# Optimization experiments

Hardware: AMD Instinct MI355X
Metric: run time of the kernel (lower is better)

The kernel has to match this reference:

```python
import jax, jax.numpy as jnp
import numpy as np

EMBED_DIM = 300
HIDDEN = 128
N_CLS = 20
N_NODES = 100000
N_EDGES = 1600000
N_GRAPHS = 512
EPSILON = 1e-06


def setup_inputs() -> dict:
    key = jax.random.key(0)
    ks = jax.random.split(key, 10)
    x_fp16 = jax.random.normal(ks[0], (N_NODES, EMBED_DIM), dtype=jnp.float16)
    ei = jax.random.randint(ks[1], (2, N_EDGES), 0, N_NODES, dtype=jnp.int32)
    batch = jnp.sort(jax.random.randint(ks[2], (N_NODES,), 0, N_GRAPHS, dtype=jnp.int32))
    mask = jax.random.randint(ks[3], (N_NODES,), 0, 2, dtype=jnp.int32).astype(jnp.bool_)
    def glorot(k, fan_in, fan_out):
        s = (6.0 / (fan_in + fan_out)) ** 0.5
        return jax.random.uniform(k, (fan_in, fan_out), jnp.float32, -s, s)
    return {
        "x_fp16": x_fp16, "ei": ei, "batch": batch, "mask": mask,
        "W1": glorot(ks[4], EMBED_DIM, HIDDEN), "b1": jnp.zeros((HIDDEN,), jnp.float32),
        "W2": glorot(ks[5], HIDDEN, HIDDEN), "b2": jnp.zeros((HIDDEN,), jnp.float32),
        "Wout": glorot(ks[6], HIDDEN, N_CLS), "bout": jnp.zeros((N_CLS,), jnp.float32),
    }


def gcn_conv(x, W, b, src, dst, n):
    # PyG GCNConv: x' = D^{-1/2} (A + I) D^{-1/2} (x W) + b
    h = x @ W  # [N, out]
    loop = jnp.arange(n, dtype=src.dtype)
    s = jnp.concatenate([src, loop])
    d = jnp.concatenate([dst, loop])
    deg = jax.ops.segment_sum(jnp.ones_like(d, dtype=h.dtype), d, num_segments=n)
    dinv = jax.lax.rsqrt(deg)  # deg >= 1 thanks to self-loops
    norm = dinv[s] * dinv[d]  # [E+N]
    msg = h[s] * norm[:, None]
    return jax.ops.segment_sum(msg, d, num_segments=n) + b


def reference(x_fp16, ei, batch, mask, W1, b1, W2, b2, Wout, bout):
    n = x_fp16.shape[0]
    src, dst = ei[0], ei[1]
    x = x_fp16.astype(jnp.float32)
    x = jax.nn.relu(gcn_conv(x, W1, b1, src, dst, n))
    x = jax.nn.relu(gcn_conv(x, W2, b2, src, dst, n))
    m = mask.astype(jnp.float32)[:, None]  # [N,1]
    ent_sum = jax.ops.segment_sum(x * m, batch, num_segments=N_GRAPHS)  # [G,H]
    ent_cnt = jax.ops.segment_sum(m, batch, num_segments=N_GRAPHS)  # [G,1]
    doc_vec = ent_sum / (ent_cnt + EPSILON)
    # fallback: mean over all nodes when a graph has no masked entities
    node_sum = jax.ops.segment_sum(x, batch, num_segments=N_GRAPHS)
    node_cnt = jax.ops.segment_sum(jnp.ones((n, 1), jnp.float32), batch, num_segments=N_GRAPHS)
    mean_pool = node_sum / jnp.maximum(node_cnt, 1.0)
    zero = ent_cnt < EPSILON  # [G,1]
    doc_vec = jnp.where(zero, mean_pool, doc_vec)
    return jax.nn.log_softmax(doc_vec @ Wout + bout, axis=1)
```

## Files before the change

kernel.cpp:

```cpp
#include <hip/hip_runtime.h>
#include <hip/hip_fp16.h>

#define NN 100000
#define NE 1600000
#define DIM 300
#define HID 128
#define NC 20
#define NG 512
#define NBK 196
#define BCH 4096

typedef _Float16 h8 __attribute__((ext_vector_type(8)));
typedef float f4 __attribute__((ext_vector_type(4)));

union pack16 { float4 v; __half2 h2[4]; };

__device__ __forceinline__ __half tohalf(float v) {
  if (!(v == v)) v = 0.f;
  v = fminf(fmaxf(v, -60000.f), 60000.f);
  return __float2half(v);
}

__device__ __forceinline__ float load_x(const void* xraw, size_t o, int mode) {
  float v;
  if (mode == 2) v = ((const float*)xraw)[o];
  else {
    unsigned short u = ((const unsigned short*)xraw)[o];
    if (mode == 1) { union { unsigned w; float f; } c; c.w = ((unsigned)u) << 16; v = c.f; }
    else { union { unsigned short s; _Float16 h; } c; c.s = u; v = (float)c.h; }
  }
  if (!(v == v)) v = 0.f;
  return fminf(fmaxf(v, -1e4f), 1e4f);
}

__device__ __forceinline__ void cvt4(const void* Ain, size_t off, int mode, _Float16* o) {
  if (mode == 2) {
    float4 fv = *(const float4*)((const float*)Ain + off);
    o[0] = (_Float16)fv.x; o[1] = (_Float16)fv.y; o[2] = (_Float16)fv.z; o[3] = (_Float16)fv.w;
  } else {
    uint2 u = *(const uint2*)((const unsigned short*)Ain + off);
    unsigned short s0 = u.x & 0xFFFF, s1 = u.x >> 16, s2 = u.y & 0xFFFF, s3 = u.y >> 16;
    if (mode == 1) {
      union { unsigned w; float f; } c0, c1, c2, c3;
      c0.w = ((unsigned)s0) << 16; c1.w = ((unsigned)s1) << 16;
      c2.w = ((unsigned)s2) << 16; c3.w = ((unsigned)s3) << 16;
      o[0] = (_Float16)c0.f; o[1] = (_Float16)c1.f; o[2] = (_Float16)c2.f; o[3] = (_Float16)c3.f;
    } else {
      union { unsigned short s; _Float16 h; } d0, d1, d2, d3;
      d0.s = s0; d1.s = s1; d2.s = s2; d3.s = s3;
      o[0] = d0.h; o[1] = d1.h; o[2] = d2.h; o[3] = d3.h;
    }
  }
}


__global__ void k_probe(const unsigned short* __restrict__ xu,
                        const unsigned* __restrict__ Araw, const unsigned* __restrict__ Braw,
                        const int* __restrict__ e32,
                        const float* __restrict__ W1, const float* __restrict__ W2,
                        _Float16* __restrict__ w1f, _Float16* __restrict__ w2f,
                        unsigned* __restrict__ diag) {
  int b = blockIdx.x, t = threadIdx.x;
  if (b < 96) {
    int mode = b % 3, chunk = b / 3;
    float m = 0.f;
    if (mode == 0) {
      int base = chunk * 16384;
      for (int j = t; j < 16384; j += 256) {
        union { unsigned short s; _Float16 h; } c; c.s = xu[base + j];
        float v = fabsf((float)c.h);
        if (v == v && v < 65000.f) m = fmaxf(m, v);
      }
    } else if (mode == 1) {
      int base = chunk * 16384;
      for (int j = t; j < 16384; j += 256) {
        union { unsigned w; float f; } c; c.w = ((unsigned)xu[base + j]) << 16;
        float v = fabsf(c.f);
        if (v == v && v < 1e30f) m = fmaxf(m, v);
      }
    } else {
      const float* xf = (const float*)xu;
      int base = chunk * 8192;
      for (int j = t; j < 8192; j += 256) {
        float v = fabsf(xf[base + j]);
        if (v == v && v < 1e30f) m = fmaxf(m, v);
      }
    }
    for (int off = 32; off; off >>= 1) m = fmaxf(m, __shfl_xor(m, off));
    if ((t & 63) == 0) atomicMax(&diag[20 + mode], __float_as_uint(m));
  } else if (b == 96 || b == 97) {
    __shared__ unsigned red[256];
    const unsigned* p = (b == 96) ? Araw : Braw;
    unsigned m = 0;
    for (int j = t; j < 25000; j += 256) m = max(m, p[j]);
    red[t] = m; __syncthreads();
    for (int off = 128; off; off >>= 1) { if (t < off) red[t] = max(red[t], red[t + off]); __syncthreads(); }
    if (t == 0) diag[(b == 96) ? 24 : 25] = red[0];
  } else if (b < 102) {
    int i = (b - 98) * 256 + t;
    unsigned z = 0;
    for (; i < 50000; i += 1024) if (e32[2 * i + 1] == 0) z++;
    for (int off = 32; off; off >>= 1) z += __shfl_xor(z, off);
    if ((t & 63) == 0) atomicAdd(&diag[26], z);
  } else {
    int idx = (b - 102) * 256 + t;
    const int S1 = 10 * 8 * 64 * 8;
    const int S2 = 4 * 8 * 64 * 8;
    if (idx < S1) {
      int j = idx & 7, l = (idx >> 3) & 63, nt = (idx >> 9) & 7, kc = idx >> 12;
      int k = kc * 32 + ((l >> 4) << 3) + j;
      int n = nt * 16 + (l & 15);
      w1f[idx] = (k < DIM) ? (_Float16)W1[k * HID + n] : (_Float16)0.f;
    } else if (idx < S1 + S2) {
      int q = idx - S1;
      int j = q & 7, l = (q >> 3) & 63, nt = (q >> 9) & 7, kc = q >> 12;
      int k = kc * 32 + ((l >> 4) << 3) + j;
      int n = nt * 16 + (l & 15);
      w2f[q] = (_Float16)W2[k * HID + n];
    }
  }
}


__global__ void k_setup(const unsigned* __restrict__ diag, int* __restrict__ flags,
                        const int* __restrict__ A, const int* __restrict__ B,
                        int* __restrict__ bcnt, int* __restrict__ gstart) {
  __shared__ int sflags[8];
  int t = threadIdx.x;
  if (t == 0) {
    float M16 = __uint_as_float(diag[20]);
    float M32 = __uint_as_float(diag[21]);
    float Mf  = __uint_as_float(diag[22]);
    int xmode = 3;
    if      (Mf  > 3.f && Mf  < 8.f) xmode = 2;
    else if (M32 > 3.f && M32 < 8.f) xmode = 1;
    else if (M16 > 3.f && M16 < 8.f) xmode = 0;
    unsigned uA = diag[24], uB = diag[25];
    bool Ab = (uA >= 32u && uA < 1024u), Bb = (uB >= 32u && uB < 1024u);
    int swap = -1;
    if (Ab && !Bb) swap = 0;
    else if (Bb && !Ab) swap = 1;
    int mint = -1;
    if (swap >= 0) {
      unsigned um = (swap == 0) ? uB : uA;
      if (um <= 1u) mint = 1;
      else if (um >= 65536u) mint = 0;
    }
    sflags[0] = xmode;
    sflags[1] = (mint == 1) ? 1 : 0;
    sflags[2] = (swap == 1) ? 1 : 0;
    sflags[3] = (diag[26] >= 49990u) ? 1 : 0;
    sflags[4] = (swap >= 0 && mint >= 0) ? 1 : 0;
    #pragma unroll
    for (int j = 0; j < 5; j++) flags[j] = sflags[j];
  }
  __syncthreads();
  const int* batch = sflags[2] ? B : A;
  if (t <= NG) {
    if (t == NG) gstart[NG] = NN;
    else {
      int lo = 0, hi = NN;
      while (lo < hi) { int mid = (lo + hi) >> 1; if (batch[mid] < t) lo = mid + 1; else hi = mid; }
      gstart[t] = lo;
    }
  }
  if (t < NBK) bcnt[t] = 0;
}


__global__ void k_bhist(const int* __restrict__ e32, const int* __restrict__ flags,
                        int* __restrict__ bcnt) {
  __shared__ int hist[NBK];
  int e64 = flags[3];
  int t = threadIdx.x;
  for (int j = t; j < NBK; j += 256) hist[j] = 0;
  __syncthreads();
  int i = blockIdx.x * blockDim.x + t;
  int stride = gridDim.x * blockDim.x;
  for (; i < NE; i += stride) {
    int s = e64 ? e32[2 * i] : e32[i];
    int d = e64 ? e32[2 * NE + 2 * i] : e32[NE + i];
    if ((unsigned)s < (unsigned)NN && (unsigned)d < (unsigned)NN)
      atomicAdd(&hist[d >> 9], 1);
  }
  __syncthreads();
  for (int j = t; j < NBK; j += 256) if (hist[j]) atomicAdd(&bcnt[j], hist[j]);
}

__global__ void k_bscan(const int* __restrict__ bcnt, int* __restrict__ boff,
                        int* __restrict__ bcur) {
  if (blockIdx.x == 0 && threadIdx.x == 0) {
    int run = 0;
    for (int j = 0; j < NBK; j++) { boff[j] = run; bcur[j] = run; run += bcnt[j]; }
    boff[NBK] = run;
  }
}

__global__ __launch_bounds__(256)
void k_bscatter(const int* __restrict__ e32, const int* __restrict__ flags,
                int* __restrict__ bcur, unsigned* __restrict__ ebuf) {
  __shared__ uint2 stage[BCH];
  __shared__ int hist[NBK];
  __shared__ int lbase[NBK];
  __shared__ int lcur[NBK];
  int e64 = flags[3];
  int t = threadIdx.x;
  for (int j = t; j < NBK; j += 256) { hist[j] = 0; lcur[j] = 0; }
  __syncthreads();
  int start = blockIdx.x * BCH;
  int n = NE - start; if (n > BCH) n = BCH;
  for (int i = t; i < n; i += 256) {
    int idx = start + i;
    int s = e64 ? e32[2 * idx] : e32[idx];
    int d = e64 ? e32[2 * NE + 2 * idx] : e32[NE + idx];
    bool ok = ((unsigned)s < (unsigned)NN) && ((unsigned)d < (unsigned)NN);
    stage[i] = make_uint2(ok ? (unsigned)s : 0xFFFFFFFFu, (unsigned)(ok ? d : 0));
    if (ok) atomicAdd(&hist[d >> 9], 1);
  }
  __syncthreads();
  for (int j = t; j < NBK; j += 256) if (hist[j] > 0) lbase[j] = atomicAdd(&bcur[j], hist[j]);
  __syncthreads();
  for (int i = t; i < n; i += 256) {
    unsigned s = stage[i].x;
    if (s == 0xFFFFFFFFu) continue;
    int d = (int)stage[i].y;
    int b = d >> 9;
    int o = atomicAdd(&lcur[b], 1);
    ebuf[lbase[b] + o] = (s << 9) | (unsigned)(d & 511);
  }
}

__global__ __launch_bounds__(256)
void k_bfinal(const unsigned* __restrict__ ebuf, const int* __restrict__ boff,
              int* __restrict__ row_off, float* __restrict__ dinv, int* __restrict__ csr) {
  __shared__ int ldeg[512];
  __shared__ int lcur[512];
  int b = blockIdx.x, t = threadIdx.x;
  int base = b * 512;
  int nn = NN - base; if (nn > 512) nn = 512;
  for (int j = t; j < 512; j += 256) ldeg[j] = 0;
  __syncthreads();
  int s0 = boff[b], s1 = boff[b + 1];
  for (int e = s0 + t; e < s1; e += 256) atomicAdd(&ldeg[ebuf[e] & 511], 1);
  __syncthreads();
  if (t == 0) {
    int run = s0;
    for (int i = 0; i < nn; i++) { lcur[i] = run; row_off[base + i] = run; run += ldeg[i]; }
    if (b == gridDim.x - 1) row_off[NN] = run;
  }
  __syncthreads();
  for (int j = t; j < nn; j += 256) dinv[base + j] = rsqrtf((float)ldeg[j] + 1.0f);
  for (int e = s0 + t; e < s1; e += 256) {
    unsigned v = ebuf[e];
    int p = atomicAdd(&lcur[v & 511], 1);
    csr[p] = (int)(v >> 9);
  }
}


#define XS1 168

__global__ __launch_bounds__(512)
void k_gemm1_mfma(const void* __restrict__ Ain, const _Float16* __restrict__ bfrag,
                  const float* __restrict__ dinv, const int* __restrict__ flags,
                  __half* __restrict__ outg) {
  __shared__ _Float16 xs[64 * XS1];
  const int mode = flags[0] & 3;
  int tid = threadIdx.x;
  int w = tid >> 6, l = tid & 63;
  int rowbase = blockIdx.x * 64;
  int k0base = (l >> 4) << 3;
  int cb = l & 15;

  f4 acc[4];
  f4 zero = {0.f, 0.f, 0.f, 0.f};
  #pragma unroll
  for (int rg = 0; rg < 4; rg++) acc[rg] = zero;

  #pragma unroll
  for (int it = 0; it < 5; it++) {
    int c = tid + it * 512;
    int rl = c / 40, kk = (c - rl * 40) * 4;
    int r = rowbase + rl;
    _Float16 o[4] = {0, 0, 0, 0};
    if (r < NN) cvt4(Ain, (size_t)r * DIM + kk, mode, o);
    _Float16* p = &xs[rl * XS1 + kk];
    p[0] = o[0]; p[1] = o[1]; p[2] = o[2]; p[3] = o[3];
  }
  __syncthreads();
  #pragma unroll
  for (int kc = 0; kc < 5; kc++) {
    int ko = kc * 32 + k0base;
    h8 a0 = *(const h8*)&xs[(0 * 16 + cb) * XS1 + ko];
    h8 a1 = *(const h8*)&xs[(1 * 16 + cb) * XS1 + ko];
    h8 a2 = *(const h8*)&xs[(2 * 16 + cb) * XS1 + ko];
    h8 a3 = *(const h8*)&xs[(3 * 16 + cb) * XS1 + ko];
    h8 bv = *(const h8*)&bfrag[(((kc << 3) + w) * 64 + l) * 8];
    acc[0] = __builtin_amdgcn_mfma_f32_16x16x32_f16(a0, bv, acc[0], 0, 0, 0);
    acc[1] = __builtin_amdgcn_mfma_f32_16x16x32_f16(a1, bv, acc[1], 0, 0, 0);
    acc[2] = __builtin_amdgcn_mfma_f32_16x16x32_f16(a2, bv, acc[2], 0, 0, 0);
    acc[3] = __builtin_amdgcn_mfma_f32_16x16x32_f16(a3, bv, acc[3], 0, 0, 0);
  }
  __syncthreads();

  for (int t2 = tid; t2 < 64 * 10; t2 += 512) {
    int rl = t2 / 10, j = t2 - rl * 10;
    *(unsigned*)&xs[rl * XS1 + 140 + j * 2] = 0u;
  }
  #pragma unroll
  for (int it = 0; it < 5; it++) {
    int c = tid + it * 512;
    if (c < 64 * 35) {
      int rl = c / 35, kk = (c - rl * 35) * 4;
      int r = rowbase + rl;
      _Float16 o[4] = {0, 0, 0, 0};
      if (r < NN) cvt4(Ain, (size_t)r * DIM + 160 + kk, mode, o);
      _Float16* p = &xs[rl * XS1 + kk];
      p[0] = o[0]; p[1] = o[1]; p[2] = o[2]; p[3] = o[3];
    }
  }
  __syncthreads();
  #pragma unroll
  for (int kc = 5; kc < 10; kc++) {
    int ko = (kc - 5) * 32 + k0base;
    h8 a0 = *(const h8*)&xs[(0 * 16 + cb) * XS1 + ko];
    h8 a1 = *(const h8*)&xs[(1 * 16 + cb) * XS1 + ko];
    h8 a2 = *(const h8*)&xs[(2 * 16 + cb) * XS1 + ko];
    h8 a3 = *(const h8*)&xs[(3 * 16 + cb) * XS1 + ko];
    h8 bv = *(const h8*)&bfrag[(((kc << 3) + w) * 64 + l) * 8];
    acc[0] = __builtin_amdgcn_mfma_f32_16x16x32_f16(a0, bv, acc[0], 0, 0, 0);
    acc[1] = __builtin_amdgcn_mfma_f32_16x16x32_f16(a1, bv, acc[1], 0, 0, 0);
    acc[2] = __builtin_amdgcn_mfma_f32_16x16x32_f16(a2, bv, acc[2], 0, 0, 0);
    acc[3] = __builtin_amdgcn_mfma_f32_16x16x32_f16(a3, bv, acc[3], 0, 0, 0);
  }

  int rquad = (l >> 4) << 2;
  #pragma unroll
  for (int rg = 0; rg < 4; rg++) {
    #pragma unroll
    for (int i = 0; i < 4; i++) {
      int r = rowbase + rg * 16 + rquad + i;
      if (r >= NN) continue;
      float dv = dinv[r];
      outg[(size_t)r * HID + w * 16 + cb] = tohalf(acc[rg][i] * dv);
    }
  }
}


__global__ __launch_bounds__(256)
void k_gemm2_mfma(const __half* __restrict__ Ain, const _Float16* __restrict__ bfrag,
                  const float* __restrict__ dinv, __half* __restrict__ outg) {
  __shared__ _Float16 xs[64 * 136];
  int tid = threadIdx.x;
  int w = tid >> 6, l = tid & 63;
  int rowbase = blockIdx.x * 64;
  int k0base = (l >> 4) << 3;
  int cb = l & 15;

  {
    h8 regs[4];
    #pragma unroll
    for (int it = 0; it < 4; it++) {
      int c = tid + it * 256;
      int rl = c >> 4, k = (c & 15) * 8;
      int r = rowbase + rl;
      h8 v = {};
      if (r < NN) v = *(const h8*)((const _Float16*)Ain + (size_t)r * HID + k);
      regs[it] = v;
    }
    __builtin_amdgcn_sched_barrier(0);
    #pragma unroll
    for (int it = 0; it < 4; it++) {
      int c = tid + it * 256;
      int rl = c >> 4, k = (c & 15) * 8;
      *(h8*)&xs[rl * 136 + k] = regs[it];
    }
  }
  __syncthreads();

  f4 acc[4][2];
  f4 zero = {0.f, 0.f, 0.f, 0.f};
  #pragma unroll
  for (int rg = 0; rg < 4; rg++) { acc[rg][0] = zero; acc[rg][1] = zero; }

  #pragma unroll
  for (int kc = 0; kc < 4; kc++) {
    int ko = kc * 32 + k0base;
    h8 a0 = *(const h8*)&xs[(0 * 16 + cb) * 136 + ko];
    h8 a1 = *(const h8*)&xs[(1 * 16 + cb) * 136 + ko];
    h8 a2 = *(const h8*)&xs[(2 * 16 + cb) * 136 + ko];
    h8 a3 = *(const h8*)&xs[(3 * 16 + cb) * 136 + ko];
    #pragma unroll
    for (int ntl = 0; ntl < 2; ntl++) {
      int nt = w * 2 + ntl;
      h8 bv = *(const h8*)&bfrag[(((kc << 3) + nt) * 64 + l) * 8];
      acc[0][ntl] = __builtin_amdgcn_mfma_f32_16x16x32_f16(a0, bv, acc[0][ntl], 0, 0, 0);
      acc[1][ntl] = __builtin_amdgcn_mfma_f32_16x16x32_f16(a1, bv, acc[1][ntl], 0, 0, 0);
      acc[2][ntl] = __builtin_amdgcn_mfma_f32_16x16x32_f16(a2, bv, acc[2][ntl], 0, 0, 0);
      acc[3][ntl] = __builtin_amdgcn_mfma_f32_16x16x32_f16(a3, bv, acc[3][ntl], 0, 0, 0);
    }
  }

  int rquad = (l >> 4) << 2;
  #pragma unroll
  for (int rg = 0; rg < 4; rg++) {
    #pragma unroll
    for (int i = 0; i < 4; i++) {
      int r = rowbase + rg * 16 + rquad + i;
      if (r >= NN) continue;
      float dv = dinv[r];
      __half* orow = outg + (size_t)r * HID;
      orow[(w * 2 + 0) * 16 + cb] = tohalf(acc[rg][0][i] * dv);
      orow[(w * 2 + 1) * 16 + cb] = tohalf(acc[rg][1][i] * dv);
    }
  }
}


__global__ __launch_bounds__(256)
void k_agg(const __half* __restrict__ g, const float* __restrict__ dinv,
           const int* __restrict__ row_off, const int* __restrict__ csr,
           const float* __restrict__ bias, __half* __restrict__ out) {
  int tid = threadIdx.x;
  int node = blockIdx.x * 4 + (tid >> 6);
  int l = tid & 63;
  if (node >= NN) return;
  int grp = l >> 4;
  int cl  = l & 15;
  size_t coff = (size_t)cl * 8;

  float a0 = 0.f, a1 = 0.f, a2 = 0.f, a3 = 0.f, a4 = 0.f, a5 = 0.f, a6 = 0.f, a7 = 0.f;
  pack16 r;

  #define ACCUM() do { \
    float2 f0 = __half22float2(r.h2[0]); \
    float2 f1 = __half22float2(r.h2[1]); \
    float2 f2 = __half22float2(r.h2[2]); \
    float2 f3 = __half22float2(r.h2[3]); \
    a0 += f0.x; a1 += f0.y; a2 += f1.x; a3 += f1.y; \
    a4 += f2.x; a5 += f2.y; a6 += f3.x; a7 += f3.y; } while (0)

  int e0 = row_off[node], e1 = row_off[node + 1];
  int e = e0 + grp;
  for (; e + 4 < e1; e += 8) {
    int s1 = csr[e], s2 = csr[e + 4];
    pack16 rA, rB;
    rA.v = *(const float4*)(g + (size_t)s1 * HID + coff);
    rB.v = *(const float4*)(g + (size_t)s2 * HID + coff);
    r = rA; ACCUM();
    r = rB; ACCUM();
  }
  if (e < e1) {
    int s1 = csr[e];
    r.v = *(const float4*)(g + (size_t)s1 * HID + coff);
    ACCUM();
  }
  if (grp == 0) {
    r.v = *(const float4*)(g + (size_t)node * HID + coff);
    ACCUM();
  }
  #undef ACCUM

  a0 += __shfl_xor(a0, 16); a1 += __shfl_xor(a1, 16); a2 += __shfl_xor(a2, 16); a3 += __shfl_xor(a3, 16);
  a4 += __shfl_xor(a4, 16); a5 += __shfl_xor(a5, 16); a6 += __shfl_xor(a6, 16); a7 += __shfl_xor(a7, 16);
  a0 += __shfl_xor(a0, 32); a1 += __shfl_xor(a1, 32); a2 += __shfl_xor(a2, 32); a3 += __shfl_xor(a3, 32);
  a4 += __shfl_xor(a4, 32); a5 += __shfl_xor(a5, 32); a6 += __shfl_xor(a6, 32); a7 += __shfl_xor(a7, 32);

  if (grp == 0) {
    float di = dinv[node];
    const float* bp = bias + coff;
    pack16 w;
    w.h2[0] = __floats2half2_rn(fmaxf(a0 * di + bp[0], 0.f), fmaxf(a1 * di + bp[1], 0.f));
    w.h2[1] = __floats2half2_rn(fmaxf(a2 * di + bp[2], 0.f), fmaxf(a3 * di + bp[3], 0.f));
    w.h2[2] = __floats2half2_rn(fmaxf(a4 * di + bp[4], 0.f), fmaxf(a5 * di + bp[5], 0.f));
    w.h2[3] = __floats2half2_rn(fmaxf(a6 * di + bp[6], 0.f), fmaxf(a7 * di + bp[7], 0.f));
    *(float4*)(out + (size_t)node * HID + coff) = w.v;
  }
}


__global__ __launch_bounds__(256)
void k_pool(const __half* __restrict__ o2, const void* __restrict__ Araw, const void* __restrict__ Braw,
            const int* __restrict__ gstart, const int* __restrict__ flags,
            float* __restrict__ doc) {
  __shared__ float lex[4][HID];
  __shared__ float lnx[4][HID];
  __shared__ int lec[4];
  int gid = blockIdx.x, tid = threadIdx.x;
  int wv = tid >> 6, l = tid & 63;
  int grp = l >> 4, cl = l & 15;
  size_t coff = (size_t)cl * 8;
  const int mint = flags[1];
  const void* mraw = flags[2] ? Araw : Braw;
  const unsigned char* m8 = (const unsigned char*)mraw;
  const int* m32 = (const int*)mraw;
  int s = gstart[gid], e = gstart[gid + 1];

  float ex[8], nx[8];
  #pragma unroll
  for (int j = 0; j < 8; j++) { ex[j] = 0.f; nx[j] = 0.f; }
  int ec = 0;

  for (int n = s + wv * 4 + grp; n < e; n += 16) {
    pack16 r;
    r.v = *(const float4*)(o2 + (size_t)n * HID + coff);
    float2 f0 = __half22float2(r.h2[0]);
    float2 f1 = __half22float2(r.h2[1]);
    float2 f2 = __half22float2(r.h2[2]);
    float2 f3 = __half22float2(r.h2[3]);
    float t0 = f0.x, t1 = f0.y, t2 = f1.x, t3 = f1.y;
    float t4 = f2.x, t5 = f2.y, t6 = f3.x, t7 = f3.y;
    nx[0] += t0; nx[1] += t1; nx[2] += t2; nx[3] += t3;
    nx[4] += t4; nx[5] += t5; nx[6] += t6; nx[7] += t7;
    bool mv = mint ? (m32[n] != 0) : (m8[n] != 0);
    if (mv) {
      ex[0] += t0; ex[1] += t1; ex[2] += t2; ex[3] += t3;
      ex[4] += t4; ex[5] += t5; ex[6] += t6; ex[7] += t7;
      ec++;
    }
  }
  #pragma unroll
  for (int j = 0; j < 8; j++) {
    ex[j] += __shfl_xor(ex[j], 16); ex[j] += __shfl_xor(ex[j], 32);
    nx[j] += __shfl_xor(nx[j], 16); nx[j] += __shfl_xor(nx[j], 32);
  }
  ec += __shfl_xor(ec, 16); ec += __shfl_xor(ec, 32);

  if (grp == 0) {
    #pragma unroll
    for (int j = 0; j < 8; j++) { lex[wv][cl * 8 + j] = ex[j]; lnx[wv][cl * 8 + j] = nx[j]; }
    if (cl == 0) lec[wv] = ec;
  }
  __syncthreads();
  if (tid < HID) {
    float exT = lex[0][tid] + lex[1][tid] + lex[2][tid] + lex[3][tid];
    float nxT = lnx[0][tid] + lnx[1][tid] + lnx[2][tid] + lnx[3][tid];
    int ecT = lec[0] + lec[1] + lec[2] + lec[3];
    int cnt = e - s;
    float dv;
    if (ecT > 0) dv = exT / ((float)ecT + 1e-6f);
    else dv = (cnt > 0) ? nxT / (float)cnt : 0.f;
    doc[gid * HID + tid] = dv;
  }
}

__global__ __launch_bounds__(64)
void k_out(const float* __restrict__ doc, const float* __restrict__ Wout,
           const float* __restrict__ bout, float* __restrict__ out) {
  __shared__ float dv[HID];
  int gid = blockIdx.x, l = threadIdx.x;
  dv[l] = doc[gid * HID + l];
  dv[l + 64] = doc[gid * HID + l + 64];
  __syncthreads();
  float logit = -1e30f;
  if (l < NC) {
    float acc = bout[l];
    for (int k = 0; k < HID; k++) acc += dv[k] * Wout[k * NC + l];
    logit = acc;
  }
  float m = logit;
  for (int off = 32; off; off >>= 1) m = fmaxf(m, __shfl_xor(m, off));
  float ex = (l < NC) ? expf(logit - m) : 0.f;
  float ssum = ex;
  for (int off = 32; off; off >>= 1) ssum += __shfl_xor(ssum, off);
  if (l < NC) out[gid * NC + l] = (logit - m) - logf(ssum);
}

__global__ void k_fail(float* __restrict__ out, float enc) {
  int i = blockIdx.x * blockDim.x + threadIdx.x;
  if (i < NG * NC) out[i] = -enc;
}


extern "C" void kernel_launch(void* const* d_in, const int* in_sizes, int n_in,
                              void* d_out, int out_size, void* d_ws, size_t ws_size,
                              hipStream_t stream) {
  int ix = -1, iei = -1, iA = -1, iB = -1, iW1 = -1, ib1 = -1, iW2 = -1, ib2 = -1, iWo = -1, ibo = -1;
  for (int i = 0; i < n_in; i++) {
    int s = in_sizes[i];
    if (s == 30000000) ix = i;
    else if (s == 3200000) iei = i;
    else if (s == 100000) { if (iA < 0) iA = i; else iB = i; }
    else if (s == 38400) iW1 = i;
    else if (s == 16384) iW2 = i;
    else if (s == 2560) iWo = i;
    else if (s == 20) ibo = i;
    else if (s == 128) { if (ib1 < 0) ib1 = i; else ib2 = i; }
  }
  float* out = (float*)d_out;
  int miss = -1;
  if (ix < 0) miss = 0; else if (iei < 0) miss = 1; else if (iA < 0 || iB < 0) miss = 2;
  else if (iW1 < 0) miss = 3; else if (ib1 < 0 || ib2 < 0) miss = 4; else if (iW2 < 0) miss = 5;
  else if (iWo < 0) miss = 6; else if (ibo < 0) miss = 7;
  if (miss >= 0) {
    k_fail<<<(NG * NC + 255) / 256, 256, 0, stream>>>(out, 8192.f + 64.f * (float)miss);
    return;
  }
  const void* x = d_in[ix];
  const int* e32 = (const int*)d_in[iei];
  const void* Araw = d_in[iA];
  const void* Braw = d_in[iB];
  const float* W1 = (const float*)d_in[iW1];
  const float* b1 = (const float*)d_in[ib1];
  const float* W2 = (const float*)d_in[iW2];
  const float* b2 = (const float*)d_in[ib2];
  const float* Wout = (const float*)d_in[iWo];
  const float* bout = (const float*)d_in[ibo];

  char* ws = (char*)d_ws;
  size_t off = 0;
  auto alloc = [&](size_t bytes) -> char* {
    char* p = ws + off; off += (bytes + 255) & ~(size_t)255; return p;
  };
  float* dinv   = (float*)alloc((size_t)NN * 4);
  int* row_off  = (int*)alloc((size_t)(NN + 1) * 4);
  int* csr      = (int*)alloc((size_t)NE * 4);
  int* bcnt     = (int*)alloc((size_t)NBK * 4);
  int* boff     = (int*)alloc((size_t)(NBK + 1) * 4);
  int* bcur     = (int*)alloc((size_t)NBK * 4);
  int* gstart   = (int*)alloc((size_t)(NG + 1) * 4);
  int* flags    = (int*)alloc(8 * 4);
  _Float16* w1f = (_Float16*)alloc(40960 * 2);
  _Float16* w2f = (_Float16*)alloc(16384 * 2);
  __half* gbuf  = (__half*)alloc((size_t)NN * HID * 2);
  __half* obuf  = (__half*)alloc((size_t)NN * HID * 2);
  float* doc    = (float*)alloc((size_t)NG * HID * 4);
  unsigned* diag = (unsigned*)alloc(64 * 4);
  unsigned* ebuf = (unsigned*)gbuf;

  hipMemsetAsync(diag, 0, 64 * 4, stream);

  k_probe<<<326, 256, 0, stream>>>((const unsigned short*)x, (const unsigned*)Araw,
                                   (const unsigned*)Braw, e32, W1, W2, w1f, w2f, diag);
  k_setup<<<1, 576, 0, stream>>>(diag, flags, (const int*)Araw, (const int*)Braw, bcnt, gstart);

  k_bhist<<<1024, 256, 0, stream>>>(e32, flags, bcnt);
  k_bscan<<<1, 64, 0, stream>>>(bcnt, boff, bcur);
  k_bscatter<<<(NE + BCH - 1) / BCH, 256, 0, stream>>>(e32, flags, bcur, ebuf);
  k_bfinal<<<NBK, 256, 0, stream>>>(ebuf, boff, row_off, dinv, csr);

  k_gemm1_mfma<<<(NN + 63) / 64, 512, 0, stream>>>(x, w1f, dinv, flags, gbuf);
  k_agg<<<NN / 4, 256, 0, stream>>>(gbuf, dinv, row_off, csr, b1, obuf);
  k_gemm2_mfma<<<(NN + 63) / 64, 256, 0, stream>>>(obuf, w2f, dinv, gbuf);
  k_agg<<<NN / 4, 256, 0, stream>>>(gbuf, dinv, row_off, csr, b2, obuf);

  k_pool<<<NG, 256, 0, stream>>>(obuf, Araw, Braw, gstart, flags, doc);
  k_out<<<NG, 64, 0, stream>>>(doc, Wout, bout, out);
}
```

Measured before the change: 309.0 us.

## Fuse layer-1 aggregation into GEMM2, fold scan into histogram, fuse pooling with output head

The first aggregation now runs inside the GEMM2 kernel: each 64-row block gathers neighbour features into shared memory and then runs the MFMA tiles from there, so the aggregated layer-1 activations are never written to or re-read from global memory. The bucket prefix scan moves into the last finishing block of the histogram kernel, coordinated by an atomic counter. The pooling and classifier/log-softmax kernels are merged. Together these drop three launches and one full intermediate round trip, but the fused kernel has only about 1563 blocks doing irregular gathers, which may lower parallelism and latency hiding compared with the separate aggregation kernel.

```diff
diff --git a/kernel.cpp b/kernel.cpp
--- a/kernel.cpp
+++ b/kernel.cpp
@@ -169,7 +169,8 @@
 
 
 __global__ void k_bhist(const int* __restrict__ e32, const int* __restrict__ flags,
-                        int* __restrict__ bcnt) {
+                        int* __restrict__ bcnt, int* __restrict__ boff,
+                        int* __restrict__ bcur, unsigned* __restrict__ done) {
   __shared__ int hist[NBK];
   int e64 = flags[3];
   int t = threadIdx.x;
@@ -185,14 +186,14 @@
   }
   __syncthreads();
   for (int j = t; j < NBK; j += 256) if (hist[j]) atomicAdd(&bcnt[j], hist[j]);
-}
-
-__global__ void k_bscan(const int* __restrict__ bcnt, int* __restrict__ boff,
-                        int* __restrict__ bcur) {
-  if (blockIdx.x == 0 && threadIdx.x == 0) {
-    int run = 0;
-    for (int j = 0; j < NBK; j++) { boff[j] = run; bcur[j] = run; run += bcnt[j]; }
-    boff[NBK] = run;
+  __threadfence();
+  __syncthreads();
+  if (t == 0) {
+    if (atomicAdd(done, 1u) == gridDim.x - 1) {
+      int run = 0;
+      for (int j = 0; j < NBK; j++) { boff[j] = run; bcur[j] = run; run += bcnt[j]; }
+      boff[NBK] = run;
+    }
   }
 }
 
@@ -349,36 +350,78 @@
 
 
 __global__ __launch_bounds__(256)
-void k_gemm2_mfma(const __half* __restrict__ Ain, const _Float16* __restrict__ bfrag,
-                  const float* __restrict__ dinv, __half* __restrict__ outg) {
+void k_aggemm2(const __half* __restrict__ g, const float* __restrict__ dinv,
+               const int* __restrict__ row_off, const int* __restrict__ csr,
+               const float* __restrict__ bias, const _Float16* __restrict__ bfrag,
+               __half* __restrict__ outg) {
   __shared__ _Float16 xs[64 * 136];
   int tid = threadIdx.x;
   int w = tid >> 6, l = tid & 63;
   int rowbase = blockIdx.x * 64;
+  int grp = l >> 4;
+  int cl  = l & 15;
+  size_t coff = (size_t)cl * 8;
+
+  for (int it = 0; it < 16; it++) {
+    int nloc = it * 4 + w;
+    int node = rowbase + nloc;
+    float a0 = 0.f, a1 = 0.f, a2 = 0.f, a3 = 0.f, a4 = 0.f, a5 = 0.f, a6 = 0.f, a7 = 0.f;
+    pack16 r;
+
+    #define ACCUM() do { \
+      float2 f0 = __half22float2(r.h2[0]); \
+      float2 f1 = __half22float2(r.h2[1]); \
+      float2 f2 = __half22float2(r.h2[2]); \
+      float2 f3 = __half22float2(r.h2[3]); \
+      a0 += f0.x; a1 += f0.y; a2 += f1.x; a3 += f1.y; \
+      a4 += f2.x; a5 += f2.y; a6 += f3.x; a7 += f3.y; } while (0)
+
+    int e0 = 0, e1 = 0;
+    if (node < NN) { e0 = row_off[node]; e1 = row_off[node + 1]; }
+    int e = e0 + grp;
+    for (; e + 4 < e1; e += 8) {
+      int s1 = csr[e], s2 = csr[e + 4];
+      pack16 rA, rB;
+      rA.v = *(const float4*)(g + (size_t)s1 * HID + coff);
+      rB.v = *(const float4*)(g + (size_t)s2 * HID + coff);
+      r = rA; ACCUM();
+      r = rB; ACCUM();
+    }
+    if (e < e1) {
+      int s1 = csr[e];
+      r.v = *(const float4*)(g + (size_t)s1 * HID + coff);
+      ACCUM();
+    }
+    if (grp == 0 && node < NN) {
+      r.v = *(const float4*)(g + (size_t)node * HID + coff);
+      ACCUM();
+    }
+    #undef ACCUM
+
+    a0 += __shfl_xor(a0, 16); a1 += __shfl_xor(a1, 16); a2 += __shfl_xor(a2, 16); a3 += __shfl_xor(a3, 16);
+    a4 += __shfl_xor(a4, 16); a5 += __shfl_xor(a5, 16); a6 += __shfl_xor(a6, 16); a7 += __shfl_xor(a7, 16);
+    a0 += __shfl_xor(a0, 32); a1 += __shfl_xor(a1, 32); a2 += __shfl_xor(a2, 32); a3 += __shfl_xor(a3, 32);
+    a4 += __shfl_xor(a4, 32); a5 += __shfl_xor(a5, 32); a6 += __shfl_xor(a6, 32); a7 += __shfl_xor(a7, 32);
+
+    if (grp == 0) {
+      pack16 wv;
+      if (node < NN) {
+        float di = dinv[node];
+        const float* bp = bias + coff;
+        wv.h2[0] = __floats2half2_rn(fmaxf(a0 * di + bp[0], 0.f), fmaxf(a1 * di + bp[1], 0.f));
+        wv.h2[1] = __floats2half2_rn(fmaxf(a2 * di + bp[2], 0.f), fmaxf(a3 * di + bp[3], 0.f));
+        wv.h2[2] = __floats2half2_rn(fmaxf(a4 * di + bp[4], 0.f), fmaxf(a5 * di + bp[5], 0.f));
+        wv.h2[3] = __floats2half2_rn(fmaxf(a6 * di + bp[6], 0.f), fmaxf(a7 * di + bp[7], 0.f));
+      } else {
+        wv.v = make_float4(0.f, 0.f, 0.f, 0.f);
+      }
+      *(float4*)&xs[nloc * 136 + cl * 8] = wv.v;
+    }
+  }
+  __syncthreads();
+
   int k0base = (l >> 4) << 3;
   int cb = l & 15;
-
-  {
-    h8 regs[4];
-    #pragma unroll
-    for (int it = 0; it < 4; it++) {
-      int c = tid + it * 256;
-      int rl = c >> 4, k = (c & 15) * 8;
-      int r = rowbase + rl;
-      h8 v = {};
-      if (r < NN) v = *(const h8*)((const _Float16*)Ain + (size_t)r * HID + k);
-      regs[it] = v;
-    }
-    __builtin_amdgcn_sched_barrier(0);
-    #pragma unroll
-    for (int it = 0; it < 4; it++) {
-      int c = tid + it * 256;
-      int rl = c >> 4, k = (c & 15) * 8;
-      *(h8*)&xs[rl * 136 + k] = regs[it];
-    }
-  }
-  __syncthreads();
-
   f4 acc[4][2];
   f4 zero = {0.f, 0.f, 0.f, 0.f};
   #pragma unroll
@@ -483,10 +526,12 @@
 __global__ __launch_bounds__(256)
 void k_pool(const __half* __restrict__ o2, const void* __restrict__ Araw, const void* __restrict__ Braw,
             const int* __restrict__ gstart, const int* __restrict__ flags,
-            float* __restrict__ doc) {
+            const float* __restrict__ Wout, const float* __restrict__ bout,
+            float* __restrict__ out) {
   __shared__ float lex[4][HID];
   __shared__ float lnx[4][HID];
   __shared__ int lec[4];
+  __shared__ float ldoc[HID];
   int gid = blockIdx.x, tid = threadIdx.x;
   int wv = tid >> 6, l = tid & 63;
   int grp = l >> 4, cl = l & 15;
@@ -541,30 +586,23 @@
     float dv;
     if (ecT > 0) dv = exT / ((float)ecT + 1e-6f);
     else dv = (cnt > 0) ? nxT / (float)cnt : 0.f;
-    doc[gid * HID + tid] = dv;
-  }
-}
-
-__global__ __launch_bounds__(64)
-void k_out(const float* __restrict__ doc, const float* __restrict__ Wout,
-           const float* __restrict__ bout, float* __restrict__ out) {
-  __shared__ float dv[HID];
-  int gid = blockIdx.x, l = threadIdx.x;
-  dv[l] = doc[gid * HID + l];
-  dv[l + 64] = doc[gid * HID + l + 64];
-  __syncthreads();
-  float logit = -1e30f;
-  if (l < NC) {
-    float acc = bout[l];
-    for (int k = 0; k < HID; k++) acc += dv[k] * Wout[k * NC + l];
-    logit = acc;
-  }
-  float m = logit;
-  for (int off = 32; off; off >>= 1) m = fmaxf(m, __shfl_xor(m, off));
-  float ex = (l < NC) ? expf(logit - m) : 0.f;
-  float ssum = ex;
-  for (int off = 32; off; off >>= 1) ssum += __shfl_xor(ssum, off);
-  if (l < NC) out[gid * NC + l] = (logit - m) - logf(ssum);
+    ldoc[tid] = dv;
+  }
+  __syncthreads();
+  if (tid < 64) {
+    float logit = -1e30f;
+    if (tid < NC) {
+      float acc = bout[tid];
+      for (int k = 0; k < HID; k++) acc += ldoc[k] * Wout[k * NC + tid];
+      logit = acc;
+    }
+    float m = logit;
+    for (int off = 32; off; off >>= 1) m = fmaxf(m, __shfl_xor(m, off));
+    float exv = (tid < NC) ? expf(logit - m) : 0.f;
+    float ssum = exv;
+    for (int off = 32; off; off >>= 1) ssum += __shfl_xor(ssum, off);
+    if (tid < NC) out[gid * NC + tid] = (logit - m) - logf(ssum);
+  }
 }
 
 __global__ void k_fail(float* __restrict__ out, float enc) {
@@ -625,7 +663,6 @@
   _Float16* w2f = (_Float16*)alloc(16384 * 2);
   __half* gbuf  = (__half*)alloc((size_t)NN * HID * 2);
   __half* obuf  = (__half*)alloc((size_t)NN * HID * 2);
-  float* doc    = (float*)alloc((size_t)NG * HID * 4);
   unsigned* diag = (unsigned*)alloc(64 * 4);
   unsigned* ebuf = (unsigned*)gbuf;
 
@@ -635,16 +672,13 @@
                                    (const unsigned*)Braw, e32, W1, W2, w1f, w2f, diag);
   k_setup<<<1, 576, 0, stream>>>(diag, flags, (const int*)Araw, (const int*)Braw, bcnt, gstart);
 
-  k_bhist<<<1024, 256, 0, stream>>>(e32, flags, bcnt);
-  k_bscan<<<1, 64, 0, stream>>>(bcnt, boff, bcur);
+  k_bhist<<<1024, 256, 0, stream>>>(e32, flags, bcnt, boff, bcur, &diag[32]);
   k_bscatter<<<(NE + BCH - 1) / BCH, 256, 0, stream>>>(e32, flags, bcur, ebuf);
   k_bfinal<<<NBK, 256, 0, stream>>>(ebuf, boff, row_off, dinv, csr);
 
   k_gemm1_mfma<<<(NN + 63) / 64, 512, 0, stream>>>(x, w1f, dinv, flags, gbuf);
-  k_agg<<<NN / 4, 256, 0, stream>>>(gbuf, dinv, row_off, csr, b1, obuf);
-  k_gemm2_mfma<<<(NN + 63) / 64, 256, 0, stream>>>(obuf, w2f, dinv, gbuf);
-  k_agg<<<NN / 4, 256, 0, stream>>>(gbuf, dinv, row_off, csr, b2, obuf);
-
-  k_pool<<<NG, 256, 0, stream>>>(obuf, Araw, Braw, gstart, flags, doc);
-  k_out<<<NG, 64, 0, stream>>>(doc, Wout, bout, out);
-}
+  k_aggemm2<<<(NN + 63) / 64, 256, 0, stream>>>(gbuf, dinv, row_off, csr, b1, w2f, obuf);
+  k_agg<<<NN / 4, 256, 0, stream>>>(obuf, dinv, row_off, csr, b2, gbuf);
+
+  k_pool<<<NG, 256, 0, stream>>>(gbuf, Araw, Braw, gstart, flags, Wout, bout, out);
+}
```

New measurement: 379.5 us. 1.23x slower.
